# Performance work log

Hardware: AMD Instinct MI355X
Metric: run time of the kernel (lower is better)

Reference implementation:

```python
import jax, jax.numpy as jnp
import numpy as np

B, S, D_IN, D_OUT, N_HEAD = 4, 2048, 1024, 1024, 16
D_HEAD = D_OUT // N_HEAD


def setup_inputs() -> dict:
    key = jax.random.key(0)
    k_x, k_wq, k_wo, k_bo = jax.random.split(key, 4)
    x = jax.random.normal(k_x, (B, S, D_IN), dtype=jnp.float32)
    # nn.Linear(d_in, d_out) weight is [d_out, d_in]; we store transposed [d_in, d_out]
    W_Q = jax.random.normal(k_wq, (D_IN, D_OUT), dtype=jnp.float32) * (D_IN ** -0.5)
    W_out = jax.random.normal(k_wo, (D_OUT, D_OUT), dtype=jnp.float32) * (D_OUT ** -0.5)
    b_out = jax.random.normal(k_bo, (D_OUT,), dtype=jnp.float32) * 0.01
    return {"x": x, "W_Q": W_Q, "W_out": W_out, "b_out": b_out}


def reference(x, W_Q, W_out, b_out):
    b, n_tok, _ = x.shape
    # Faithful to source: Q, K, V all use W_Q (source bug preserved)
    qkv = jnp.einsum('btd,de->bte', x, W_Q)  # [b, s, d_out]
    q = qkv.reshape(b, n_tok, N_HEAD, D_HEAD).transpose(0, 2, 1, 3)  # [b,h,s,dh]
    k = q
    v = q
    scores = jnp.einsum('bhqd,bhkd->bhqk', q, k)  # [b,h,s,s]
    causal = jnp.triu(jnp.ones((n_tok, n_tok), dtype=bool), k=1)
    scores = jnp.where(causal, -jnp.inf, scores)
    # source divides by sqrt(d_head) after masking; -inf / c == -inf so same result
    attn = jax.nn.softmax(scores / jnp.sqrt(jnp.float32(D_HEAD)), axis=-1)
    ctx = jnp.einsum('bhqk,bhkd->bhqd', attn, v)  # [b,h,s,dh]
    ctx = ctx.transpose(0, 2, 1, 3).reshape(b, n_tok, D_OUT)
    return jnp.einsum('btd,de->bte', ctx, W_out) + b_out
```

## Files before the change

### kernel.cpp

```cpp
#include <hip/hip_runtime.h>
#include <hip/hip_bf16.h>
#include <math.h>

#define B_ 4
#define S_ 2048
#define NH_ 16
#define DH_ 64
#define DM_ 1024

typedef __attribute__((ext_vector_type(4))) float f32x4;
typedef __attribute__((ext_vector_type(8))) short s16x8;
typedef __attribute__((ext_vector_type(4))) short s16x4;
typedef __attribute__((ext_vector_type(2))) unsigned u32x2;

extern "C" __device__ float __ocml_native_exp2_f32(float);
static __device__ __forceinline__ float nexp2(float x) {
  return __ocml_native_exp2_f32(x);
}

static __device__ __forceinline__ short f2bf(float f) {
  union { float f; unsigned u; } c; c.f = f;
  unsigned r = c.u + 0x7fffu + ((c.u >> 16) & 1u);
  return (short)(r >> 16);
}

static __device__ __forceinline__ unsigned pkbf_fast(float a, float b) {
  unsigned r;
  asm("v_cvt_pk_bf16_f32 %0, %1, %2" : "=v"(r) : "v"(a), "v"(b));
  return r;
}

static __device__ __forceinline__ s16x4 mk4(unsigned lo, unsigned hi) {
  union { unsigned u[2]; s16x4 v; } x; x.u[0] = lo; x.u[1] = hi; return x.v;
}

#if __has_builtin(__builtin_amdgcn_mfma_f32_16x16x16bf16_1k)
#define HAVE16 1
static __device__ __forceinline__ f32x4 pv_mfma(s16x4 a, s16x4 b, f32x4 c) {
  return __builtin_amdgcn_mfma_f32_16x16x16bf16_1k(a, b, c, 0, 0, 0);
}
#else
#define HAVE16 0
static __device__ __forceinline__ f32x4 pv_mfma(s16x4 a, s16x4 b, f32x4 c) {
  asm volatile("v_mfma_f32_16x16x16_bf16 %0, %1, %2, %0" : "+v"(c) : "v"(a), "v"(b));
  return c;
}
#endif

static __device__ __forceinline__ void gload16(const void* g, void* l) {
  __builtin_amdgcn_global_load_lds(
      (const __attribute__((address_space(1))) void*)g,
      (__attribute__((address_space(3))) void*)l, 16, 0, 0);
}

__global__ void cvt_kernel(const float* __restrict__ in, short* __restrict__ out) {
  int i = (blockIdx.x * 256 + threadIdx.x) * 8;
  f32x4 a = *(const f32x4*)(in + i);
  f32x4 b = *(const f32x4*)(in + i + 4);
  s16x8 o;
  o[0] = f2bf(a[0]); o[1] = f2bf(a[1]); o[2] = f2bf(a[2]); o[3] = f2bf(a[3]);
  o[4] = f2bf(b[0]); o[5] = f2bf(b[1]); o[6] = f2bf(b[2]); o[7] = f2bf(b[3]);
  *(s16x8*)(out + i) = o;
}

__global__ void tcvt_kernel(const float* __restrict__ W0, const float* __restrict__ W1,
                            short* __restrict__ T0, short* __restrict__ T1) {
  __shared__ float t[32][33];
  const float* W = blockIdx.z ? W1 : W0;
  short* WT = blockIdx.z ? T1 : T0;
  int tx = threadIdx.x & 31, ty = threadIdx.x >> 5;
  int bn = blockIdx.x * 32, bk = blockIdx.y * 32;
#pragma unroll
  for (int r = 0; r < 32; r += 8)
    t[ty + r][tx] = W[(size_t)(bk + ty + r) * DM_ + bn + tx];
  __syncthreads();
#pragma unroll
  for (int r = 0; r < 32; r += 8)
    WT[(size_t)(bn + ty + r) * DM_ + bk + tx] = f2bf(t[tx][ty + r]);
}

template <int EPI>
__global__ __launch_bounds__(256, 4) void gemm_kernel(
    const short* __restrict__ A, const short* __restrict__ BT,
    void* __restrict__ Cout, short* __restrict__ CoutT,
    const float* __restrict__ bias) {
  __shared__ short Al[64 * 64];
  __shared__ short Bl[128 * 64];
  const int tid = threadIdx.x;
  const int wid = tid >> 6, lane = tid & 63;
  const int l15 = lane & 15, l4 = lane >> 4;
  const int bm = blockIdx.y * 64, bn = blockIdx.x * 128;
  const int wm = (wid >> 1) * 32, wn = (wid & 1) * 64;
  f32x4 acc[2][4] = {};

  for (int kt = 0; kt < DM_; kt += 64) {
    __syncthreads();
#pragma unroll
    for (int j = 0; j < 2; ++j) {
      int s = j * 256 + tid;
      int row = s >> 3;
      int sl = (s & 7) ^ (row & 7);
      gload16(A + (size_t)(bm + row) * DM_ + kt + sl * 8, &Al[j * 2048 + wid * 512]);
    }
#pragma unroll
    for (int j = 0; j < 4; ++j) {
      int s = j * 256 + tid;
      int row = s >> 3;
      int sl = (s & 7) ^ (row & 7);
      gload16(BT + (size_t)(bn + row) * DM_ + kt + sl * 8, &Bl[j * 2048 + wid * 512]);
    }
    __syncthreads();
#pragma unroll
    for (int kk = 0; kk < 2; ++kk) {
      s16x8 af[2], bfr[4];
#pragma unroll
      for (int mi = 0; mi < 2; ++mi) {
        int row = wm + mi * 16 + l15;
        int sl = (kk * 4 + l4) ^ (row & 7);
        af[mi] = *(const s16x8*)&Al[row * 64 + sl * 8];
      }
#pragma unroll
      for (int ni = 0; ni < 4; ++ni) {
        int row = wn + ni * 16 + l15;
        int sl = (kk * 4 + l4) ^ (row & 7);
        bfr[ni] = *(const s16x8*)&Bl[row * 64 + sl * 8];
      }
#pragma unroll
      for (int mi = 0; mi < 2; ++mi)
#pragma unroll
        for (int ni = 0; ni < 4; ++ni)
          acc[mi][ni] = __builtin_amdgcn_mfma_f32_16x16x32_bf16(af[mi], bfr[ni], acc[mi][ni], 0, 0, 0);
    }
  }

  if (EPI == 0) {
    const float sc = 0.42466089786f;
    short* Q = (short*)Cout;
#pragma unroll
    for (int mi = 0; mi < 2; ++mi)
#pragma unroll
      for (int ni = 0; ni < 4; ++ni) {
        int rr0 = bm + wm + mi * 16 + l4 * 4;
        int cc = bn + wn + ni * 16 + l15;
        int b = rr0 >> 11, s0 = rr0 & 2047, h = cc >> 6, d = cc & 63;
        int bh = b * NH_ + h;
        u32x2 pk;
        pk[0] = pkbf_fast(acc[mi][ni][0] * sc, acc[mi][ni][1] * sc);
        pk[1] = pkbf_fast(acc[mi][ni][2] * sc, acc[mi][ni][3] * sc);
        Q[(((size_t)bh * S_ + s0 + 0) << 6) + d] = (short)(pk[0] & 0xffff);
        Q[(((size_t)bh * S_ + s0 + 1) << 6) + d] = (short)(pk[0] >> 16);
        Q[(((size_t)bh * S_ + s0 + 2) << 6) + d] = (short)(pk[1] & 0xffff);
        Q[(((size_t)bh * S_ + s0 + 3) << 6) + d] = (short)(pk[1] >> 16);
        *(u32x2*)&CoutT[(((size_t)bh * DH_ + d) << 11) + s0] = pk;
      }
  } else {
    float* O = (float*)Cout;
#pragma unroll
    for (int mi = 0; mi < 2; ++mi)
#pragma unroll
      for (int ni = 0; ni < 4; ++ni)
#pragma unroll
        for (int r = 0; r < 4; ++r) {
          int rr = bm + wm + mi * 16 + l4 * 4 + r;
          int cc = bn + wn + ni * 16 + l15;
          O[(size_t)rr * DM_ + cc] = acc[mi][ni][r] + bias[cc];
        }
  }
}

__global__ __launch_bounds__(256, 4) void attn_kernel(
    const short* __restrict__ Qb, const short* __restrict__ QbT,
    short* __restrict__ Ctx) {
  __shared__ short Kl[2][64 * 64];
  __shared__ short Vt[2][64 * 64];
  const int tid = threadIdx.x;
  const int wid = tid >> 6, lane = tid & 63;
  const int l15 = lane & 15, l4 = lane >> 4;
  const int bid = blockIdx.x;
  const int bh = bid & 63;
  const int g = bid >> 6;
  const int qt = (int)((0x32104567ba98cdefULL >> (g * 4)) & 15);
  const short* Qh = Qb + (size_t)bh * S_ * DH_;
  const short* QTh = QbT + (size_t)bh * DH_ * S_;
  const int q0 = qt * 128 + wid * 32;

  s16x8 aq[2][2];
#pragma unroll
  for (int qi = 0; qi < 2; ++qi)
#pragma unroll
    for (int kk = 0; kk < 2; ++kk)
      aq[qi][kk] = *(const s16x8*)(Qh + (size_t)(q0 + qi * 16 + l15) * DH_ + kk * 32 + l4 * 8);

  f32x4 acc_o[4][2] = {};
  f32x4 lacc[2] = {};
  s16x4 ones;
  ones[0] = (short)0x3F80; ones[1] = (short)0x3F80;
  ones[2] = (short)0x3F80; ones[3] = (short)0x3F80;

  const int e7 = l15 & 7;
  const int ka0 = l15 * 64 + ((l4) ^ e7) * 8;
  const int ka1 = l15 * 64 + ((4 + l4) ^ e7) * 8;
  int vtoff[4];
#pragma unroll
  for (int ki = 0; ki < 4; ++ki)
    vtoff[ki] = l15 * 64 + (((ki * 2 + (l4 >> 1)) ^ e7) << 3) + (l4 & 1) * 4;

  const int c0 = wid * 64 + lane, c1 = c0 + 256;
  const int r0 = c0 >> 3, s0 = (c0 & 7) ^ (r0 & 7);
  const int r1 = c1 >> 3, s1 = (c1 & 7) ^ (r1 & 7);
  const short* pK0 = Qh + r0 * 64 + s0 * 8;
  const short* pK1 = Qh + r1 * 64 + s1 * 8;
  const short* pV0 = QTh + (size_t)r0 * S_ + s0 * 8;
  const short* pV1 = QTh + (size_t)r1 * S_ + s1 * 8;

  auto stage = [&](int buf) {
    gload16(pK0, &Kl[buf][wid * 512]);
    gload16(pK1, &Kl[buf][wid * 512 + 2048]);
    gload16(pV0, &Vt[buf][wid * 512]);
    gload16(pV1, &Vt[buf][wid * 512 + 2048]);
    pK0 += 4096; pK1 += 4096;
    pV0 += 64;   pV1 += 64;
  };

  stage(0);

  int cur = 0;
  const int nt = qt * 2 + 2;
  for (int t = 0; t < nt; ++t) {
    asm volatile("s_waitcnt vmcnt(0)" ::: "memory");
    __syncthreads();
    if (t + 1 < nt) stage(cur ^ 1);
    const int kv0 = t * 64;

    if (kv0 <= q0) {
      const short* kl = &Kl[cur][0];
      const short* vt = &Vt[cur][0];
      f32x4 sa[4][2] = {};
      __builtin_amdgcn_s_setprio(1);
#pragma unroll
      for (int kk = 0; kk < 2; ++kk) {
        const int kb = (kk == 0) ? ka0 : ka1;
        s16x8 ka[4];
#pragma unroll
        for (int ki = 0; ki < 4; ++ki)
          ka[ki] = *(const s16x8*)&kl[kb + ki * 1024];
#pragma unroll
        for (int ki = 0; ki < 4; ++ki)
#pragma unroll
          for (int qi = 0; qi < 2; ++qi)
            sa[ki][qi] = __builtin_amdgcn_mfma_f32_16x16x32_bf16(ka[ki], aq[qi][kk], sa[ki][qi], 0, 0, 0);
      }
      __builtin_amdgcn_s_setprio(0);
      if (kv0 + 63 > q0) {
#pragma unroll
        for (int ki = 0; ki < 4; ++ki)
#pragma unroll
          for (int qi = 0; qi < 2; ++qi)
#pragma unroll
            for (int r = 0; r < 4; ++r) {
              int kvg = kv0 + ki * 16 + l4 * 4 + r;
              int qg = q0 + qi * 16 + l15;
              if (kvg > qg) sa[ki][qi][r] = -INFINITY;
            }
      }
      unsigned pw[4][2][2];
#pragma unroll
      for (int ki = 0; ki < 4; ++ki)
#pragma unroll
        for (int qi = 0; qi < 2; ++qi) {
          float e0 = nexp2(sa[ki][qi][0]);
          float e1 = nexp2(sa[ki][qi][1]);
          float e2 = nexp2(sa[ki][qi][2]);
          float e3 = nexp2(sa[ki][qi][3]);
          pw[ki][qi][0] = pkbf_fast(e0, e1);
          pw[ki][qi][1] = pkbf_fast(e2, e3);
        }
      __builtin_amdgcn_s_setprio(1);
#pragma unroll
      for (int ki = 0; ki < 4; ++ki) {
        lacc[0] = pv_mfma(ones, mk4(pw[ki][0][0], pw[ki][0][1]), lacc[0]);
        lacc[1] = pv_mfma(ones, mk4(pw[ki][1][0], pw[ki][1][1]), lacc[1]);
      }
#pragma unroll
      for (int df = 0; df < 4; ++df) {
#pragma unroll
        for (int ki = 0; ki < 4; ++ki) {
          s16x4 av = *(const s16x4*)&vt[df * 1024 + vtoff[ki]];
          acc_o[df][0] = pv_mfma(av, mk4(pw[ki][0][0], pw[ki][0][1]), acc_o[df][0]);
          acc_o[df][1] = pv_mfma(av, mk4(pw[ki][1][0], pw[ki][1][1]), acc_o[df][1]);
        }
      }
      __builtin_amdgcn_s_setprio(0);
#if !HAVE16
      asm volatile("s_nop 7" :::);
      asm volatile("s_nop 7" :::);
#endif
    }
    cur ^= 1;
  }

  const int b = bh >> 4, h = bh & 15;
  const float ISQC = 2.35482208f;
  float inv[2] = {ISQC / lacc[0][0], ISQC / lacc[1][0]};
#pragma unroll
  for (int df = 0; df < 4; ++df)
#pragma unroll
    for (int qi = 0; qi < 2; ++qi) {
      int qg = q0 + qi * 16 + l15;
      int col = h * 64 + df * 16 + l4 * 4;
      u32x2 pk;
      pk[0] = pkbf_fast(acc_o[df][qi][0] * inv[qi], acc_o[df][qi][1] * inv[qi]);
      pk[1] = pkbf_fast(acc_o[df][qi][2] * inv[qi], acc_o[df][qi][3] * inv[qi]);
      *(u32x2*)&Ctx[(size_t)(b * S_ + qg) * DM_ + col] = pk;
    }
}

extern "C" void kernel_launch(void* const* d_in, const int* in_sizes, int n_in,
                              void* d_out, int out_size, void* d_ws, size_t ws_size,
                              hipStream_t stream) {
  const float* x  = (const float*)d_in[0];
  const float* Wq = (const float*)d_in[1];
  const float* Wo = (const float*)d_in[2];
  const float* bo = (const float*)d_in[3];
  float* out = (float*)d_out;
  char* ws = (char*)d_ws;

  short* xb  = (short*)(ws);
  short* WqT = (short*)(ws + 16777216);
  short* WoT = (short*)(ws + 18874368);
  short* Qb  = (short*)(ws + 20971520);
  short* QbT = (short*)(ws + 37748736);
  short* Ctx = xb;

  cvt_kernel<<<4096, 256, 0, stream>>>(x, xb);
  tcvt_kernel<<<dim3(32, 32, 2), 256, 0, stream>>>(Wq, Wo, WqT, WoT);
  gemm_kernel<0><<<dim3(8, 128), 256, 0, stream>>>(xb, WqT, Qb, QbT, nullptr);
  attn_kernel<<<1024, 256, 0, stream>>>(Qb, QbT, Ctx);
  gemm_kernel<1><<<dim3(8, 128), 256, 0, stream>>>(Ctx, WoT, out, nullptr, bo);
}
```

Before: 124.9 us.

## Use K=32 MFMA for PV via LDS-staged P and enlarge GEMM tiles to 128x128

New measurement: 118.1 us, median of 3. 1.06x faster.

```diff
diff --git a/kernel.cpp b/kernel.cpp
--- a/kernel.cpp
+++ b/kernel.cpp
@@ -10,7 +10,6 @@
 
 typedef __attribute__((ext_vector_type(4))) float f32x4;
 typedef __attribute__((ext_vector_type(8))) short s16x8;
-typedef __attribute__((ext_vector_type(4))) short s16x4;
 typedef __attribute__((ext_vector_type(2))) unsigned u32x2;
 
 extern "C" __device__ float __ocml_native_exp2_f32(float);
@@ -29,23 +28,6 @@
   asm("v_cvt_pk_bf16_f32 %0, %1, %2" : "=v"(r) : "v"(a), "v"(b));
   return r;
 }
-
-static __device__ __forceinline__ s16x4 mk4(unsigned lo, unsigned hi) {
-  union { unsigned u[2]; s16x4 v; } x; x.u[0] = lo; x.u[1] = hi; return x.v;
-}
-
-#if __has_builtin(__builtin_amdgcn_mfma_f32_16x16x16bf16_1k)
-#define HAVE16 1
-static __device__ __forceinline__ f32x4 pv_mfma(s16x4 a, s16x4 b, f32x4 c) {
-  return __builtin_amdgcn_mfma_f32_16x16x16bf16_1k(a, b, c, 0, 0, 0);
-}
-#else
-#define HAVE16 0
-static __device__ __forceinline__ f32x4 pv_mfma(s16x4 a, s16x4 b, f32x4 c) {
-  asm volatile("v_mfma_f32_16x16x16_bf16 %0, %1, %2, %0" : "+v"(c) : "v"(a), "v"(b));
-  return c;
-}
-#endif
 
 static __device__ __forceinline__ void gload16(const void* g, void* l) {
   __builtin_amdgcn_global_load_lds(
@@ -80,23 +62,23 @@
 }
 
 template <int EPI>
-__global__ __launch_bounds__(256, 4) void gemm_kernel(
+__global__ __launch_bounds__(256, 2) void gemm_kernel(
     const short* __restrict__ A, const short* __restrict__ BT,
     void* __restrict__ Cout, short* __restrict__ CoutT,
     const float* __restrict__ bias) {
-  __shared__ short Al[64 * 64];
+  __shared__ short Al[128 * 64];
   __shared__ short Bl[128 * 64];
   const int tid = threadIdx.x;
   const int wid = tid >> 6, lane = tid & 63;
   const int l15 = lane & 15, l4 = lane >> 4;
-  const int bm = blockIdx.y * 64, bn = blockIdx.x * 128;
-  const int wm = (wid >> 1) * 32, wn = (wid & 1) * 64;
-  f32x4 acc[2][4] = {};
+  const int bm = blockIdx.y * 128, bn = blockIdx.x * 128;
+  const int wm = (wid >> 1) * 64, wn = (wid & 1) * 64;
+  f32x4 acc[4][4] = {};
 
   for (int kt = 0; kt < DM_; kt += 64) {
     __syncthreads();
 #pragma unroll
-    for (int j = 0; j < 2; ++j) {
+    for (int j = 0; j < 4; ++j) {
       int s = j * 256 + tid;
       int row = s >> 3;
       int sl = (s & 7) ^ (row & 7);
@@ -112,9 +94,9 @@
     __syncthreads();
 #pragma unroll
     for (int kk = 0; kk < 2; ++kk) {
-      s16x8 af[2], bfr[4];
-#pragma unroll
-      for (int mi = 0; mi < 2; ++mi) {
+      s16x8 af[4], bfr[4];
+#pragma unroll
+      for (int mi = 0; mi < 4; ++mi) {
         int row = wm + mi * 16 + l15;
         int sl = (kk * 4 + l4) ^ (row & 7);
         af[mi] = *(const s16x8*)&Al[row * 64 + sl * 8];
@@ -126,7 +108,7 @@
         bfr[ni] = *(const s16x8*)&Bl[row * 64 + sl * 8];
       }
 #pragma unroll
-      for (int mi = 0; mi < 2; ++mi)
+      for (int mi = 0; mi < 4; ++mi)
 #pragma unroll
         for (int ni = 0; ni < 4; ++ni)
           acc[mi][ni] = __builtin_amdgcn_mfma_f32_16x16x32_bf16(af[mi], bfr[ni], acc[mi][ni], 0, 0, 0);
@@ -137,7 +119,7 @@
     const float sc = 0.42466089786f;
     short* Q = (short*)Cout;
 #pragma unroll
-    for (int mi = 0; mi < 2; ++mi)
+    for (int mi = 0; mi < 4; ++mi)
 #pragma unroll
       for (int ni = 0; ni < 4; ++ni) {
         int rr0 = bm + wm + mi * 16 + l4 * 4;
@@ -156,7 +138,7 @@
   } else {
     float* O = (float*)Cout;
 #pragma unroll
-    for (int mi = 0; mi < 2; ++mi)
+    for (int mi = 0; mi < 4; ++mi)
 #pragma unroll
       for (int ni = 0; ni < 4; ++ni)
 #pragma unroll
@@ -173,6 +155,7 @@
     short* __restrict__ Ctx) {
   __shared__ short Kl[2][64 * 64];
   __shared__ short Vt[2][64 * 64];
+  __shared__ short Pl[4][16 * 64];
   const int tid = threadIdx.x;
   const int wid = tid >> 6, lane = tid & 63;
   const int l15 = lane & 15, l4 = lane >> 4;
@@ -193,17 +176,20 @@
 
   f32x4 acc_o[4][2] = {};
   f32x4 lacc[2] = {};
-  s16x4 ones;
-  ones[0] = (short)0x3F80; ones[1] = (short)0x3F80;
-  ones[2] = (short)0x3F80; ones[3] = (short)0x3F80;
+  s16x8 ones8;
+#pragma unroll
+  for (int i = 0; i < 8; ++i) ones8[i] = (short)0x3F80;
 
   const int e7 = l15 & 7;
   const int ka0 = l15 * 64 + ((l4) ^ e7) * 8;
   const int ka1 = l15 * 64 + ((4 + l4) ^ e7) * 8;
-  int vtoff[4];
+  const int vro0 = l15 * 64 + ((l4) ^ e7) * 8;
+  const int vro1 = l15 * 64 + ((4 + l4) ^ e7) * 8;
+  int pwo[4];
 #pragma unroll
   for (int ki = 0; ki < 4; ++ki)
-    vtoff[ki] = l15 * 64 + (((ki * 2 + (l4 >> 1)) ^ e7) << 3) + (l4 & 1) * 4;
+    pwo[ki] = l15 * 64 + (((2 * ki + (l4 >> 1)) ^ e7) << 3) + (l4 & 1) * 4;
+  const int pro0 = vro0, pro1 = vro1;
 
   const int c0 = wid * 64 + lane, c1 = c0 + 256;
   const int r0 = c0 >> 3, s0 = (c0 & 7) ^ (r0 & 7);
@@ -235,6 +221,7 @@
     if (kv0 <= q0) {
       const short* kl = &Kl[cur][0];
       const short* vt = &Vt[cur][0];
+      short* Pw = &Pl[wid][0];
       f32x4 sa[4][2] = {};
       __builtin_amdgcn_s_setprio(1);
 #pragma unroll
@@ -277,24 +264,25 @@
         }
       __builtin_amdgcn_s_setprio(1);
 #pragma unroll
-      for (int ki = 0; ki < 4; ++ki) {
-        lacc[0] = pv_mfma(ones, mk4(pw[ki][0][0], pw[ki][0][1]), lacc[0]);
-        lacc[1] = pv_mfma(ones, mk4(pw[ki][1][0], pw[ki][1][1]), lacc[1]);
-      }
-#pragma unroll
-      for (int df = 0; df < 4; ++df) {
+      for (int qi = 0; qi < 2; ++qi) {
 #pragma unroll
         for (int ki = 0; ki < 4; ++ki) {
-          s16x4 av = *(const s16x4*)&vt[df * 1024 + vtoff[ki]];
-          acc_o[df][0] = pv_mfma(av, mk4(pw[ki][0][0], pw[ki][0][1]), acc_o[df][0]);
-          acc_o[df][1] = pv_mfma(av, mk4(pw[ki][1][0], pw[ki][1][1]), acc_o[df][1]);
+          u32x2 w; w[0] = pw[ki][qi][0]; w[1] = pw[ki][qi][1];
+          *(u32x2*)&Pw[pwo[ki]] = w;
         }
+        s16x8 pb0 = *(const s16x8*)&Pw[pro0];
+        s16x8 pb1 = *(const s16x8*)&Pw[pro1];
+        lacc[qi] = __builtin_amdgcn_mfma_f32_16x16x32_bf16(ones8, pb0, lacc[qi], 0, 0, 0);
+        lacc[qi] = __builtin_amdgcn_mfma_f32_16x16x32_bf16(ones8, pb1, lacc[qi], 0, 0, 0);
+#pragma unroll
+        for (int df = 0; df < 4; ++df) {
+          s16x8 av0 = *(const s16x8*)&vt[df * 1024 + vro0];
+          s16x8 av1 = *(const s16x8*)&vt[df * 1024 + vro1];
+          acc_o[df][qi] = __builtin_amdgcn_mfma_f32_16x16x32_bf16(av0, pb0, acc_o[df][qi], 0, 0, 0);
+          acc_o[df][qi] = __builtin_amdgcn_mfma_f32_16x16x32_bf16(av1, pb1, acc_o[df][qi], 0, 0, 0);
+        }
       }
       __builtin_amdgcn_s_setprio(0);
-#if !HAVE16
-      asm volatile("s_nop 7" :::);
-      asm volatile("s_nop 7" :::);
-#endif
     }
     cur ^= 1;
   }
@@ -334,7 +322,7 @@
 
   cvt_kernel<<<4096, 256, 0, stream>>>(x, xb);
   tcvt_kernel<<<dim3(32, 32, 2), 256, 0, stream>>>(Wq, Wo, WqT, WoT);
-  gemm_kernel<0><<<dim3(8, 128), 256, 0, stream>>>(xb, WqT, Qb, QbT, nullptr);
+  gemm_kernel<0><<<dim3(8, 64), 256, 0, stream>>>(xb, WqT, Qb, QbT, nullptr);
   attn_kernel<<<1024, 256, 0, stream>>>(Qb, QbT, Ctx);
-  gemm_kernel<1><<<dim3(8, 128), 256, 0, stream>>>(Ctx, WoT, out, nullptr, bo);
-}
+  gemm_kernel<1><<<dim3(8, 64), 256, 0, stream>>>(Ctx, WoT, out, nullptr, bo);
+}
```
